# Kernel tuning notes

Measured on AMD Instinct MI355X. Metric: run time of the kernel, lower is better.

The kernel has to match this reference:

```python
import jax, jax.numpy as jnp
import numpy as np

NUM_GRAPHS = 256   # number of graph blocks in the batch
NODES = 64         # nodes per graph (PPGN uses complete pair set per graph)
C_IN = 64          # nedgeinput
C_OUT = 64         # nedgeoutput
E = NUM_GRAPHS * NODES * NODES  # total pair-edges


def _complete_edge_index():
    # PPGN edge set: all (i, j) node pairs within each graph, sorted lexicographically
    base = np.arange(NUM_GRAPHS, dtype=np.int32) * NODES
    ii = np.repeat(np.arange(NODES, dtype=np.int32), NODES)
    jj = np.tile(np.arange(NODES, dtype=np.int32), NODES)
    src = (base[:, None] + ii[None, :]).reshape(-1)
    dst = (base[:, None] + jj[None, :]).reshape(-1)
    return jnp.asarray(np.stack([src, dst]), dtype=jnp.int32)  # [2, E]


def setup_inputs() -> dict:
    key = jax.random.key(0)
    k1, k2, k3, k4 = jax.random.split(key, 4)
    edge_index = _complete_edge_index()
    SP = jax.random.normal(k1, (E, C_IN), dtype=jnp.float32)
    s = 1.0 / np.sqrt(C_IN).astype(np.float32)
    W4 = jax.random.normal(k2, (C_IN, C_IN), dtype=jnp.float32) * s   # fc1_4.weight
    W5 = jax.random.normal(k3, (C_IN, C_IN), dtype=jnp.float32) * s   # fc1_5.weight
    W6 = jax.random.normal(k4, (C_OUT, 2 * C_IN), dtype=jnp.float32) * (1.0 / np.sqrt(2 * C_IN).astype(np.float32))  # fc1_6.weight
    return {"edge_index": edge_index, "SP": SP, "W4": W4, "W5": W5, "W6": W6}


def reference(edge_index, SP, W4, W5, W6):
    # X = fc1_4(SP)/C, Y = fc1_5(SP)/C  (torch Linear: x @ W.T)
    X = (SP @ W4.T) / C_IN   # [E, C]
    Y = (SP @ W5.T) / C_IN   # [E, C]
    # block-diagonal sparse matmul per channel, restricted back to the edge pattern
    g = edge_index[0] // NODES   # graph id per edge
    il = edge_index[0] % NODES   # local row index
    jl = edge_index[1] % NODES   # local col index
    Xd = jnp.zeros((NUM_GRAPHS, NODES, NODES, C_IN), X.dtype).at[g, il, jl].set(X)
    Yd = jnp.zeros((NUM_GRAPHS, NODES, NODES, C_IN), Y.dtype).at[g, il, jl].set(Y)
    prod = jnp.einsum('bikc,bkjc->bijc', Xd, Yd)  # per-graph, per-channel matmul X @ Y
    mm = prod[g, il, jl]                           # gather back to edge list: [E, C]
    tmp = jnp.concatenate([SP, mm], axis=1)        # [E, 2C]
    return jax.nn.relu(tmp @ W6.T)                 # [E, C_OUT]
```

## Files before the change

kernel.cpp:

```cpp
#include <hip/hip_runtime.h>
#include <stdint.h>

#define NG   256
#define NN   64
#define NEDGE (NG*NN*NN)

using bf8   = __attribute__((ext_vector_type(8))) short;
using f32x4 = __attribute__((ext_vector_type(4))) float;

__device__ __forceinline__ unsigned short f2bf(float f) {
  uint32_t u = __float_as_uint(f);
  u += 0x7fffu + ((u >> 16) & 1u);
  return (unsigned short)(u >> 16);
}
__device__ __forceinline__ bf8 pk8(float4 a, float4 b) {
  bf8 r;
  r[0]=(short)f2bf(a.x); r[1]=(short)f2bf(a.y); r[2]=(short)f2bf(a.z); r[3]=(short)f2bf(a.w);
  r[4]=(short)f2bf(b.x); r[5]=(short)f2bf(b.y); r[6]=(short)f2bf(b.z); r[7]=(short)f2bf(b.w);
  return r;
}
__device__ __forceinline__ bf8 ld8bf(const float* p) {
  const float4* q = reinterpret_cast<const float4*>(p);
  return pk8(q[0], q[1]);
}
__device__ __forceinline__ bf8 u4_to_bf8(uint4 v) {
  union { uint4 u; bf8 b; } c; c.u = v; return c.b;
}

__global__ __launch_bounds__(256) void k1_xy(
    const float* __restrict__ SP, const float* __restrict__ W4,
    const float* __restrict__ W5, unsigned short* __restrict__ Xp,
    unsigned short* __restrict__ Yp)
{
  __shared__ unsigned short Wl[2][64*72];
  __shared__ unsigned short lT[2][64*72];
  const int t = threadIdx.x, w = t >> 6, lane = t & 63;
  const int lr = lane & 15, lg = lane >> 4;
  const size_t b = blockIdx.x >> 2;
  const int iq = (int)blockIdx.x & 3;

  {
    const int mat = t >> 7, row = (t >> 1) & 63, h = t & 1;
    const float* src = (mat ? W5 : W4) + row*64 + h*32;
    unsigned short* dst = Wl[mat] + row*72 + h*32;
#pragma unroll
    for (int q = 0; q < 4; ++q) {
      bf8 v = ld8bf(src + q*8);
      *reinterpret_cast<bf8*>(dst + q*8) = v;
    }
  }

#define SPADDR(it_) (SP + ((size_t)b*4096 + (size_t)(iq*16+(it_))*64 + w*16 + lr)*64 + lg*8)
#define PRELOAD(P0_,P1_,P2_,P3_, it_)                                        \
  { const float4* q = reinterpret_cast<const float4*>(SPADDR(it_));          \
    P0_ = q[0]; P1_ = q[1]; P2_ = q[8]; P3_ = q[9]; }

  float4 pA0, pA1, pA2, pA3, pB0, pB1, pB2, pB3;
  PRELOAD(pA0,pA1,pA2,pA3, 0)
  PRELOAD(pB0,pB1,pB2,pB3, 1)
  __syncthreads();

#define WFRAG(mat_, ct_, kk_)                                                \
  (*reinterpret_cast<const bf8*>(Wl[mat_] + ((ct_)*16 + lr)*72 + (kk_)*32 + lg*8))

  const float s = 0.015625f;
#define K1_W1(arr_, ct_, r_, v_)                                             \
  lT[arr_][((ct_)*16 + lg*4 + (r_))*72 + w*16 + lr] = f2bf((v_)*s);
#define K1_W(ct_, ax_, ay_)                                                  \
  K1_W1(0,ct_,0,ax_[0]) K1_W1(0,ct_,1,ax_[1])                                \
  K1_W1(0,ct_,2,ax_[2]) K1_W1(0,ct_,3,ax_[3])                                \
  K1_W1(1,ct_,0,ay_[0]) K1_W1(1,ct_,1,ay_[1])                                \
  K1_W1(1,ct_,2,ay_[2]) K1_W1(1,ct_,3,ay_[3])

#define K1_ITER(it_, P0_,P1_,P2_,P3_, NEXT_)                                 \
  {                                                                          \
    bf8 a0 = pk8(P0_, P1_);                                                  \
    bf8 a1 = pk8(P2_, P3_);                                                  \
    NEXT_                                                                    \
    f32x4 ax0={0.f,0.f,0.f,0.f}, ax1=ax0, ax2=ax0, ax3=ax0;                  \
    f32x4 ay0=ax0, ay1=ax0, ay2=ax0, ay3=ax0;                                \
    ax0 = __builtin_amdgcn_mfma_f32_16x16x32_bf16(WFRAG(0,0,0), a0, ax0,0,0,0);\
    ax0 = __builtin_amdgcn_mfma_f32_16x16x32_bf16(WFRAG(0,0,1), a1, ax0,0,0,0);\
    ay0 = __builtin_amdgcn_mfma_f32_16x16x32_bf16(WFRAG(1,0,0), a0, ay0,0,0,0);\
    ay0 = __builtin_amdgcn_mfma_f32_16x16x32_bf16(WFRAG(1,0,1), a1, ay0,0,0,0);\
    ax1 = __builtin_amdgcn_mfma_f32_16x16x32_bf16(WFRAG(0,1,0), a0, ax1,0,0,0);\
    ax1 = __builtin_amdgcn_mfma_f32_16x16x32_bf16(WFRAG(0,1,1), a1, ax1,0,0,0);\
    ay1 = __builtin_amdgcn_mfma_f32_16x16x32_bf16(WFRAG(1,1,0), a0, ay1,0,0,0);\
    ay1 = __builtin_amdgcn_mfma_f32_16x16x32_bf16(WFRAG(1,1,1), a1, ay1,0,0,0);\
    ax2 = __builtin_amdgcn_mfma_f32_16x16x32_bf16(WFRAG(0,2,0), a0, ax2,0,0,0);\
    ax2 = __builtin_amdgcn_mfma_f32_16x16x32_bf16(WFRAG(0,2,1), a1, ax2,0,0,0);\
    ay2 = __builtin_amdgcn_mfma_f32_16x16x32_bf16(WFRAG(1,2,0), a0, ay2,0,0,0);\
    ay2 = __builtin_amdgcn_mfma_f32_16x16x32_bf16(WFRAG(1,2,1), a1, ay2,0,0,0);\
    ax3 = __builtin_amdgcn_mfma_f32_16x16x32_bf16(WFRAG(0,3,0), a0, ax3,0,0,0);\
    ax3 = __builtin_amdgcn_mfma_f32_16x16x32_bf16(WFRAG(0,3,1), a1, ax3,0,0,0);\
    ay3 = __builtin_amdgcn_mfma_f32_16x16x32_bf16(WFRAG(1,3,0), a0, ay3,0,0,0);\
    ay3 = __builtin_amdgcn_mfma_f32_16x16x32_bf16(WFRAG(1,3,1), a1, ay3,0,0,0);\
    K1_W(0, ax0, ay0) K1_W(1, ax1, ay1) K1_W(2, ax2, ay2) K1_W(3, ax3, ay3)  \
    __syncthreads();                                                         \
    {                                                                        \
      const int jo = t & 7, rid = t >> 3;                                    \
      const int irow8 = (iq*16 + (it_)) * 8;                                 \
      _Pragma("unroll")                                                      \
      for (int q = 0; q < 4; ++q) {                                          \
        int row = q*32 + rid;                                                \
        int a = row >> 6, ch = row & 63;                                     \
        const unsigned short* p = lT[a] + ch*72 + jo*8;                      \
        uint2 lo = *reinterpret_cast<const uint2*>(p);                       \
        uint2 hi = *reinterpret_cast<const uint2*>(p + 4);                   \
        uint4 v; v.x = lo.x; v.y = lo.y; v.z = hi.x; v.w = hi.y;             \
        uint4* G = reinterpret_cast<uint4*>(a ? Yp : Xp);                    \
        G[(b*64 + ch)*512 + irow8 + jo] = v;                                 \
      }                                                                      \
    }                                                                        \
    __syncthreads();                                                         \
  }

#pragma unroll 1
  for (int st = 0; st < 8; ++st) {
    const int itA = st*2, itB = st*2 + 1;
    K1_ITER(itA, pA0,pA1,pA2,pA3,
            if (st < 7) { PRELOAD(pA0,pA1,pA2,pA3, itA+2) })
    K1_ITER(itB, pB0,pB1,pB2,pB3,
            if (st < 7) { PRELOAD(pB0,pB1,pB2,pB3, itB+2) })
  }
}

__global__ __launch_bounds__(256) void k2_mfma(
    const unsigned short* __restrict__ Xp, const unsigned short* __restrict__ Yp,
    unsigned short* __restrict__ mmh)
{
  __shared__ unsigned short Ys[2][64*68];
  __shared__ unsigned short Ds[2][64*68];
  const int t = threadIdx.x, w = t >> 6, lane = t & 63;
  const int lr = lane & 15, lg = lane >> 4;
  const int bid = ((int)blockIdx.x & 7) * 1024 + ((int)blockIdx.x >> 3);
  const int pw = w >> 1;
  const int mh = w & 1;
  const int plane = bid*2 + pw;

  {
    const uint4* Yg = reinterpret_cast<const uint4*>(Yp) + (size_t)plane*512;
    unsigned short* ys = Ys[pw];
    const int kk = lane >> 3, jo = lane & 7;
#pragma unroll
    for (int it = 0; it < 4; ++it) {
      int row = mh*32 + it*8 + kk;
      uint4 v = Yg[row*8 + jo];
      *reinterpret_cast<uint2*>(ys + row*68 + jo*8)     = make_uint2(v.x, v.y);
      *reinterpret_cast<uint2*>(ys + row*68 + jo*8 + 4) = make_uint2(v.z, v.w);
    }
  }
  __syncthreads();

  const unsigned short* ys = Ys[pw];
#define K2_BF(bv_, nt_, kt_)                                                 \
  bf8 bv_;                                                                   \
  bv_[0] = (short)ys[((kt_)*32 + lg*8 + 0)*68 + (nt_)*16 + lr];              \
  bv_[1] = (short)ys[((kt_)*32 + lg*8 + 1)*68 + (nt_)*16 + lr];              \
  bv_[2] = (short)ys[((kt_)*32 + lg*8 + 2)*68 + (nt_)*16 + lr];              \
  bv_[3] = (short)ys[((kt_)*32 + lg*8 + 3)*68 + (nt_)*16 + lr];              \
  bv_[4] = (short)ys[((kt_)*32 + lg*8 + 4)*68 + (nt_)*16 + lr];              \
  bv_[5] = (short)ys[((kt_)*32 + lg*8 + 5)*68 + (nt_)*16 + lr];              \
  bv_[6] = (short)ys[((kt_)*32 + lg*8 + 6)*68 + (nt_)*16 + lr];              \
  bv_[7] = (short)ys[((kt_)*32 + lg*8 + 7)*68 + (nt_)*16 + lr];
  K2_BF(b00, 0, 0) K2_BF(b01, 0, 1)
  K2_BF(b10, 1, 0) K2_BF(b11, 1, 1)
  K2_BF(b20, 2, 0) K2_BF(b21, 2, 1)
  K2_BF(b30, 3, 0) K2_BF(b31, 3, 1)

  const uint4* Xg = reinterpret_cast<const uint4*>(Xp) + (size_t)plane*512;
  f32x4 c00={0.f,0.f,0.f,0.f}, c01=c00, c02=c00, c03=c00;
  f32x4 c10=c00, c11=c00, c12=c00, c13=c00;
#define K2_MT(mt_, c0_, c1_, c2_, c3_)                                       \
  {                                                                          \
    int row = mh*32 + (mt_)*16 + lr;                                         \
    bf8 alo = u4_to_bf8(Xg[row*8 + lg]);                                     \
    bf8 ahi = u4_to_bf8(Xg[row*8 + 4 + lg]);                                 \
    c0_ = __builtin_amdgcn_mfma_f32_16x16x32_bf16(alo, b00, c0_, 0, 0, 0);   \
    c0_ = __builtin_amdgcn_mfma_f32_16x16x32_bf16(ahi, b01, c0_, 0, 0, 0);   \
    c1_ = __builtin_amdgcn_mfma_f32_16x16x32_bf16(alo, b10, c1_, 0, 0, 0);   \
    c1_ = __builtin_amdgcn_mfma_f32_16x16x32_bf16(ahi, b11, c1_, 0, 0, 0);   \
    c2_ = __builtin_amdgcn_mfma_f32_16x16x32_bf16(alo, b20, c2_, 0, 0, 0);   \
    c2_ = __builtin_amdgcn_mfma_f32_16x16x32_bf16(ahi, b21, c2_, 0, 0, 0);   \
    c3_ = __builtin_amdgcn_mfma_f32_16x16x32_bf16(alo, b30, c3_, 0, 0, 0);   \
    c3_ = __builtin_amdgcn_mfma_f32_16x16x32_bf16(ahi, b31, c3_, 0, 0, 0);   \
  }
  K2_MT(0, c00, c01, c02, c03)
  K2_MT(1, c10, c11, c12, c13)

  unsigned short* ds = Ds[pw];
#define K2_D1(mt_, nt_, r_, v_)                                              \
  ds[(mh*32 + (mt_)*16 + lg*4 + (r_))*68 + (nt_)*16 + lr] = f2bf(v_);
#define K2_D(mt_, nt_, c_)                                                   \
  K2_D1(mt_,nt_,0,c_[0]) K2_D1(mt_,nt_,1,c_[1])                              \
  K2_D1(mt_,nt_,2,c_[2]) K2_D1(mt_,nt_,3,c_[3])
  K2_D(0,0,c00) K2_D(0,1,c01) K2_D(0,2,c02) K2_D(0,3,c03)
  K2_D(1,0,c10) K2_D(1,1,c11) K2_D(1,2,c12) K2_D(1,3,c13)
  __syncthreads();

  {
    uint4* Mg = reinterpret_cast<uint4*>(mmh);
    const unsigned short* dsr = Ds[pw];
    const int kk = lane >> 3, jo = lane & 7;
    const int bb = plane >> 6, cc = plane & 63;
#pragma unroll
    for (int it = 0; it < 4; ++it) {
      int row = mh*32 + it*8 + kk;
      uint2 lo = *reinterpret_cast<const uint2*>(dsr + row*68 + jo*8);
      uint2 hi = *reinterpret_cast<const uint2*>(dsr + row*68 + jo*8 + 4);
      uint4 v; v.x = lo.x; v.y = lo.y; v.z = hi.x; v.w = hi.y;
      Mg[((size_t)bb*256 + row*4 + (jo>>1))*128 + cc*2 + (jo&1)] = v;
    }
  }
}

__global__ __launch_bounds__(256) void k3_out(
    const float* __restrict__ SP, const unsigned short* __restrict__ mmh,
    const float* __restrict__ W6, float* __restrict__ out)
{
  __shared__ unsigned short lw[64*140];
  const int t = threadIdx.x, w = t >> 6, lane = t & 63;
  const int lr = lane & 15, lg = lane >> 4;
  const size_t b = blockIdx.x >> 2;
  const int iq = (int)blockIdx.x & 3;

  {
    const int row = t >> 2, seg = t & 3;
    const float* src = W6 + row*128 + seg*32;
    unsigned short* dst = lw + row*140 + seg*32;
#pragma unroll
    for (int q = 0; q < 4; ++q) {
      bf8 v = ld8bf(src + q*8);
      *reinterpret_cast<bf8*>(dst + q*8) = v;
    }
  }

#define K3_E(idx_) (b*4096 + (size_t)(iq*16 + ((idx_)>>2)*4 + w)*64 + ((idx_)&3)*16 + lr)
#define PRELOAD3(P0_,P1_,P2_,P3_, idx_)                                      \
  { const float4* q = reinterpret_cast<const float4*>(SP + K3_E(idx_)*64 + lg*8); \
    P0_ = q[0]; P1_ = q[1]; P2_ = q[8]; P3_ = q[9]; }
#define MMLOAD(m2_, m3_, idx_)                                               \
  { const unsigned short* tp = mmh + (K3_E(idx_) >> 4)*1024 + lg*128 + lr;   \
    m2_[0]=(short)tp[0];    m2_[1]=(short)tp[16];                            \
    m2_[2]=(short)tp[32];   m2_[3]=(short)tp[48];                            \
    m2_[4]=(short)tp[64];   m2_[5]=(short)tp[80];                            \
    m2_[6]=(short)tp[96];   m2_[7]=(short)tp[112];                           \
    m3_[0]=(short)tp[512];  m3_[1]=(short)tp[528];                           \
    m3_[2]=(short)tp[544];  m3_[3]=(short)tp[560];                           \
    m3_[4]=(short)tp[576];  m3_[5]=(short)tp[592];                           \
    m3_[6]=(short)tp[608];  m3_[7]=(short)tp[624]; }

  float4 pA0, pA1, pA2, pA3, pB0, pB1, pB2, pB3;
  bf8 m2A, m3A, m2B, m3B;
  PRELOAD3(pA0,pA1,pA2,pA3, 0)
  PRELOAD3(pB0,pB1,pB2,pB3, 1)
  MMLOAD(m2A, m3A, 0)
  MMLOAD(m2B, m3B, 1)
  __syncthreads();

#define W6F(ct_, kt_)                                                        \
  (*reinterpret_cast<const bf8*>(lw + ((ct_)*16 + lr)*140 + (kt_)*32 + lg*8))

#define K3_ITER(idx_, P0_,P1_,P2_,P3_, M2_, M3_, NEXT_)                      \
  {                                                                          \
    bf8 a0 = pk8(P0_, P1_);                                                  \
    bf8 a1 = pk8(P2_, P3_);                                                  \
    bf8 a2 = M2_;                                                            \
    bf8 a3 = M3_;                                                            \
    NEXT_                                                                    \
    f32x4 c0={0.f,0.f,0.f,0.f}, c1=c0, c2=c0, c3=c0;                         \
    c0 = __builtin_amdgcn_mfma_f32_16x16x32_bf16(W6F(0,0), a0, c0, 0,0,0);   \
    c0 = __builtin_amdgcn_mfma_f32_16x16x32_bf16(W6F(0,1), a1, c0, 0,0,0);   \
    c0 = __builtin_amdgcn_mfma_f32_16x16x32_bf16(W6F(0,2), a2, c0, 0,0,0);   \
    c0 = __builtin_amdgcn_mfma_f32_16x16x32_bf16(W6F(0,3), a3, c0, 0,0,0);   \
    c1 = __builtin_amdgcn_mfma_f32_16x16x32_bf16(W6F(1,0), a0, c1, 0,0,0);   \
    c1 = __builtin_amdgcn_mfma_f32_16x16x32_bf16(W6F(1,1), a1, c1, 0,0,0);   \
    c1 = __builtin_amdgcn_mfma_f32_16x16x32_bf16(W6F(1,2), a2, c1, 0,0,0);   \
    c1 = __builtin_amdgcn_mfma_f32_16x16x32_bf16(W6F(1,3), a3, c1, 0,0,0);   \
    c2 = __builtin_amdgcn_mfma_f32_16x16x32_bf16(W6F(2,0), a0, c2, 0,0,0);   \
    c2 = __builtin_amdgcn_mfma_f32_16x16x32_bf16(W6F(2,1), a1, c2, 0,0,0);   \
    c2 = __builtin_amdgcn_mfma_f32_16x16x32_bf16(W6F(2,2), a2, c2, 0,0,0);   \
    c2 = __builtin_amdgcn_mfma_f32_16x16x32_bf16(W6F(2,3), a3, c2, 0,0,0);   \
    c3 = __builtin_amdgcn_mfma_f32_16x16x32_bf16(W6F(3,0), a0, c3, 0,0,0);   \
    c3 = __builtin_amdgcn_mfma_f32_16x16x32_bf16(W6F(3,1), a1, c3, 0,0,0);   \
    c3 = __builtin_amdgcn_mfma_f32_16x16x32_bf16(W6F(3,2), a2, c3, 0,0,0);   \
    c3 = __builtin_amdgcn_mfma_f32_16x16x32_bf16(W6F(3,3), a3, c3, 0,0,0);   \
    float* ob = out + K3_E(idx_)*64 + lg*4;                                  \
    f32x4 o;                                                                 \
    o[0]=fmaxf(c0[0],0.f); o[1]=fmaxf(c0[1],0.f);                            \
    o[2]=fmaxf(c0[2],0.f); o[3]=fmaxf(c0[3],0.f);                            \
    *reinterpret_cast<f32x4*>(ob) = o;                                       \
    o[0]=fmaxf(c1[0],0.f); o[1]=fmaxf(c1[1],0.f);                            \
    o[2]=fmaxf(c1[2],0.f); o[3]=fmaxf(c1[3],0.f);                            \
    *reinterpret_cast<f32x4*>(ob + 16) = o;                                  \
    o[0]=fmaxf(c2[0],0.f); o[1]=fmaxf(c2[1],0.f);                            \
    o[2]=fmaxf(c2[2],0.f); o[3]=fmaxf(c2[3],0.f);                            \
    *reinterpret_cast<f32x4*>(ob + 32) = o;                                  \
    o[0]=fmaxf(c3[0],0.f); o[1]=fmaxf(c3[1],0.f);                            \
    o[2]=fmaxf(c3[2],0.f); o[3]=fmaxf(c3[3],0.f);                            \
    *reinterpret_cast<f32x4*>(ob + 48) = o;                                  \
  }

#pragma unroll 1
  for (int st = 0; st < 8; ++st) {
    const int idxA = st*2, idxB = st*2 + 1;
    K3_ITER(idxA, pA0,pA1,pA2,pA3, m2A, m3A,
            if (st < 7) { PRELOAD3(pA0,pA1,pA2,pA3, idxA+2)
                          MMLOAD(m2A, m3A, idxA+2) })
    K3_ITER(idxB, pB0,pB1,pB2,pB3, m2B, m3B,
            if (st < 7) { PRELOAD3(pB0,pB1,pB2,pB3, idxB+2)
                          MMLOAD(m2B, m3B, idxB+2) })
  }
}

extern "C" void kernel_launch(void* const* d_in, const int* in_sizes, int n_in,
                              void* d_out, int out_size, void* d_ws, size_t ws_size,
                              hipStream_t stream)
{
  (void)in_sizes; (void)n_in; (void)out_size; (void)ws_size;
  const float* SP = (const float*)d_in[1];
  const float* W4 = (const float*)d_in[2];
  const float* W5 = (const float*)d_in[3];
  const float* W6 = (const float*)d_in[4];

  unsigned short* Xp = (unsigned short*)d_out;
  unsigned short* Yp = Xp + (size_t)NEDGE * 64;
  unsigned short* mmh = (unsigned short*)d_ws;
  float* out = (float*)d_out;

  k1_xy  <<<NG*4,     256, 0, stream>>>(SP, W4, W5, Xp, Yp);
  k2_mfma<<<NG*32,    256, 0, stream>>>(Xp, Yp, mmh);
  k3_out <<<NG*4,     256, 0, stream>>>(SP, mmh, W6, out);
}
```

Baseline: 337.9 us.

## Warp-specialize output kernel with producer waves staging SP through double-buffered LDS

Splits the final projection kernel into 512-thread blocks where four waves convert SP rows to bf16 into a double-buffered shared tile while four other waves load the mm tile and run the MFMA projection with ReLU. The goal is to overlap SP global loads and conversion with compute, and to coalesce SP loads. In exchange, only half the waves do MFMA work, and a block-wide barrier is added at every step.

```diff
diff --git a/kernel.cpp b/kernel.cpp
--- a/kernel.cpp
+++ b/kernel.cpp
@@ -214,33 +214,39 @@
   }
 }
 
-__global__ __launch_bounds__(256) void k3_out(
+__global__ __launch_bounds__(512) void k3_out(
     const float* __restrict__ SP, const unsigned short* __restrict__ mmh,
     const float* __restrict__ W6, float* __restrict__ out)
 {
+  __shared__ unsigned short lsp[2][64*72];
   __shared__ unsigned short lw[64*140];
   const int t = threadIdx.x, w = t >> 6, lane = t & 63;
   const int lr = lane & 15, lg = lane >> 4;
-  const size_t b = blockIdx.x >> 2;
-  const int iq = (int)blockIdx.x & 3;
+  const size_t base_e = (size_t)blockIdx.x * 512;
 
   {
-    const int row = t >> 2, seg = t & 3;
-    const float* src = W6 + row*128 + seg*32;
-    unsigned short* dst = lw + row*140 + seg*32;
-#pragma unroll
-    for (int q = 0; q < 4; ++q) {
-      bf8 v = ld8bf(src + q*8);
-      *reinterpret_cast<bf8*>(dst + q*8) = v;
-    }
-  }
-
-#define K3_E(idx_) (b*4096 + (size_t)(iq*16 + ((idx_)>>2)*4 + w)*64 + ((idx_)&3)*16 + lr)
-#define PRELOAD3(P0_,P1_,P2_,P3_, idx_)                                      \
-  { const float4* q = reinterpret_cast<const float4*>(SP + K3_E(idx_)*64 + lg*8); \
-    P0_ = q[0]; P1_ = q[1]; P2_ = q[8]; P3_ = q[9]; }
-#define MMLOAD(m2_, m3_, idx_)                                               \
-  { const unsigned short* tp = mmh + (K3_E(idx_) >> 4)*1024 + lg*128 + lr;   \
+    const int row = t >> 3, seg = t & 7;
+    bf8 v = ld8bf(W6 + row*128 + seg*16);
+    bf8 v2 = ld8bf(W6 + row*128 + seg*16 + 8);
+    *reinterpret_cast<bf8*>(lw + row*140 + seg*16) = v;
+    *reinterpret_cast<bf8*>(lw + row*140 + seg*16 + 8) = v2;
+  }
+
+#define PRODUCE(t_, buf_)                                                    \
+  {                                                                          \
+    const int e0 = t >> 3, seg = t & 7;                                      \
+    const float* s0 = SP + (base_e + (t_)*64 + e0)*64 + seg*8;               \
+    bf8 v0 = ld8bf(s0);                                                      \
+    const float* s1 = s0 + (size_t)32*64;                                    \
+    bf8 v1 = ld8bf(s1);                                                      \
+    *reinterpret_cast<bf8*>(&lsp[buf_][e0*72 + seg*8]) = v0;                 \
+    *reinterpret_cast<bf8*>(&lsp[buf_][(e0+32)*72 + seg*8]) = v1;            \
+  }
+
+  const int sub = w - 4;
+#define MMLOAD(m2_, m3_, t_)                                                 \
+  { const unsigned short* tp = mmh +                                         \
+        ((size_t)blockIdx.x*32 + (t_)*4 + sub)*1024 + lg*128 + lr;           \
     m2_[0]=(short)tp[0];    m2_[1]=(short)tp[16];                            \
     m2_[2]=(short)tp[32];   m2_[3]=(short)tp[48];                            \
     m2_[4]=(short)tp[64];   m2_[5]=(short)tp[80];                            \
@@ -250,24 +256,16 @@
     m3_[4]=(short)tp[576];  m3_[5]=(short)tp[592];                           \
     m3_[6]=(short)tp[608];  m3_[7]=(short)tp[624]; }
 
-  float4 pA0, pA1, pA2, pA3, pB0, pB1, pB2, pB3;
-  bf8 m2A, m3A, m2B, m3B;
-  PRELOAD3(pA0,pA1,pA2,pA3, 0)
-  PRELOAD3(pB0,pB1,pB2,pB3, 1)
-  MMLOAD(m2A, m3A, 0)
-  MMLOAD(m2B, m3B, 1)
-  __syncthreads();
-
 #define W6F(ct_, kt_)                                                        \
   (*reinterpret_cast<const bf8*>(lw + ((ct_)*16 + lr)*140 + (kt_)*32 + lg*8))
 
-#define K3_ITER(idx_, P0_,P1_,P2_,P3_, M2_, M3_, NEXT_)                      \
+#define CONSUME(t_, buf_, M2_, M3_)                                          \
   {                                                                          \
-    bf8 a0 = pk8(P0_, P1_);                                                  \
-    bf8 a1 = pk8(P2_, P3_);                                                  \
+    const unsigned short* sp = &lsp[buf_][(sub*16 + lr)*72 + lg*8];          \
+    bf8 a0 = *reinterpret_cast<const bf8*>(sp);                              \
+    bf8 a1 = *reinterpret_cast<const bf8*>(sp + 32);                         \
     bf8 a2 = M2_;                                                            \
     bf8 a3 = M3_;                                                            \
-    NEXT_                                                                    \
     f32x4 c0={0.f,0.f,0.f,0.f}, c1=c0, c2=c0, c3=c0;                         \
     c0 = __builtin_amdgcn_mfma_f32_16x16x32_bf16(W6F(0,0), a0, c0, 0,0,0);   \
     c0 = __builtin_amdgcn_mfma_f32_16x16x32_bf16(W6F(0,1), a1, c0, 0,0,0);   \
@@ -285,7 +283,7 @@
     c3 = __builtin_amdgcn_mfma_f32_16x16x32_bf16(W6F(3,1), a1, c3, 0,0,0);   \
     c3 = __builtin_amdgcn_mfma_f32_16x16x32_bf16(W6F(3,2), a2, c3, 0,0,0);   \
     c3 = __builtin_amdgcn_mfma_f32_16x16x32_bf16(W6F(3,3), a3, c3, 0,0,0);   \
-    float* ob = out + K3_E(idx_)*64 + lg*4;                                  \
+    float* ob = out + (base_e + (t_)*64 + sub*16 + lr)*64 + lg*4;            \
     f32x4 o;                                                                 \
     o[0]=fmaxf(c0[0],0.f); o[1]=fmaxf(c0[1],0.f);                            \
     o[2]=fmaxf(c0[2],0.f); o[3]=fmaxf(c0[3],0.f);                            \
@@ -301,15 +299,31 @@
     *reinterpret_cast<f32x4*>(ob + 48) = o;                                  \
   }
 
+  bf8 m2A, m3A, m2B, m3B;
+  if (w < 4) {
+    PRODUCE(0, 0)
+  } else {
+    MMLOAD(m2A, m3A, 0)
+  }
+  __syncthreads();
+
 #pragma unroll 1
-  for (int st = 0; st < 8; ++st) {
-    const int idxA = st*2, idxB = st*2 + 1;
-    K3_ITER(idxA, pA0,pA1,pA2,pA3, m2A, m3A,
-            if (st < 7) { PRELOAD3(pA0,pA1,pA2,pA3, idxA+2)
-                          MMLOAD(m2A, m3A, idxA+2) })
-    K3_ITER(idxB, pB0,pB1,pB2,pB3, m2B, m3B,
-            if (st < 7) { PRELOAD3(pB0,pB1,pB2,pB3, idxB+2)
-                          MMLOAD(m2B, m3B, idxB+2) })
+  for (int st = 0; st < 4; ++st) {
+    const int t0 = st*2, t1 = st*2 + 1;
+    if (w < 4) {
+      PRODUCE(t0 + 1, (t0 + 1) & 1)
+    } else {
+      MMLOAD(m2B, m3B, t1)
+      CONSUME(t0, t0 & 1, m2A, m3A)
+    }
+    __syncthreads();
+    if (w < 4) {
+      if (st < 3) { PRODUCE(t1 + 1, (t1 + 1) & 1) }
+    } else {
+      if (st < 3) { MMLOAD(m2A, m3A, t1 + 1) }
+      CONSUME(t1, t1 & 1, m2B, m3B)
+    }
+    __syncthreads();
   }
 }
 
@@ -330,5 +344,5 @@
 
   k1_xy  <<<NG*4,     256, 0, stream>>>(SP, W4, W5, Xp, Yp);
   k2_mfma<<<NG*32,    256, 0, stream>>>(Xp, Yp, mmh);
-  k3_out <<<NG*4,     256, 0, stream>>>(SP, mmh, W6, out);
-}
+  k3_out <<<NEDGE/512, 512, 0, stream>>>(SP, mmh, W6, out);
+}
```

Result: faster. 331.1 us (-2.0%).

## Stage SP tiles into LDS via async global_load_lds with double buffering in k3

Applied to the files above, without the earlier changes.

The output kernel now copies SP rows straight into a double-buffered LDS tile using global_load_lds DMA instead of holding them in registers through per-thread float4 loads. Each block processes a contiguous range of 1024 edges, and the copy of the next tile is issued while the current one is being multiplied. The aim is to cut register pressure and make the global reads coalesced and overlapped. In exchange it adds 32KB of LDS per block, which can lower occupancy, plus two block-wide barriers per tile. The layout remapping is subtle, so correctness depends on the DMA lane addressing matching the consumer indexing.

```diff
diff --git a/kernel.cpp b/kernel.cpp
--- a/kernel.cpp
+++ b/kernel.cpp
@@ -218,11 +218,11 @@
     const float* __restrict__ SP, const unsigned short* __restrict__ mmh,
     const float* __restrict__ W6, float* __restrict__ out)
 {
+  __shared__ float lsp[2][64*64];
   __shared__ unsigned short lw[64*140];
   const int t = threadIdx.x, w = t >> 6, lane = t & 63;
   const int lr = lane & 15, lg = lane >> 4;
-  const size_t b = blockIdx.x >> 2;
-  const int iq = (int)blockIdx.x & 3;
+  const size_t base_e = (size_t)blockIdx.x * 1024;
 
   {
     const int row = t >> 2, seg = t & 3;
@@ -235,12 +235,22 @@
     }
   }
 
-#define K3_E(idx_) (b*4096 + (size_t)(iq*16 + ((idx_)>>2)*4 + w)*64 + ((idx_)&3)*16 + lr)
-#define PRELOAD3(P0_,P1_,P2_,P3_, idx_)                                      \
-  { const float4* q = reinterpret_cast<const float4*>(SP + K3_E(idx_)*64 + lg*8); \
-    P0_ = q[0]; P1_ = q[1]; P2_ = q[8]; P3_ = q[9]; }
-#define MMLOAD(m2_, m3_, idx_)                                               \
-  { const unsigned short* tp = mmh + (K3_E(idx_) >> 4)*1024 + lg*128 + lr;   \
+#define K3DMA(tt_, buf_)                                                     \
+  _Pragma("unroll")                                                          \
+  for (int d = 0; d < 4; ++d) {                                              \
+    const int u = d*4 + w;                                                   \
+    const int oe = u*32 + (lane >> 1);                                       \
+    const float* src = SP + (base_e + (size_t)(tt_)*64 + (oe & 63))*64       \
+                          + (oe >> 6)*8 + (lane & 1)*4;                      \
+    __builtin_amdgcn_global_load_lds(                                        \
+        (const __attribute__((address_space(1))) unsigned int*)src,          \
+        (__attribute__((address_space(3))) unsigned int*)&lsp[buf_][u*256],  \
+        16, 0, 0);                                                           \
+  }
+
+#define MMLOAD(m2_, m3_, tt_)                                                \
+  { const unsigned short* tp = mmh +                                         \
+        ((size_t)blockIdx.x*64 + (tt_)*4 + w)*1024 + lg*128 + lr;            \
     m2_[0]=(short)tp[0];    m2_[1]=(short)tp[16];                            \
     m2_[2]=(short)tp[32];   m2_[3]=(short)tp[48];                            \
     m2_[4]=(short)tp[64];   m2_[5]=(short)tp[80];                            \
@@ -250,24 +260,16 @@
     m3_[4]=(short)tp[576];  m3_[5]=(short)tp[592];                           \
     m3_[6]=(short)tp[608];  m3_[7]=(short)tp[624]; }
 
-  float4 pA0, pA1, pA2, pA3, pB0, pB1, pB2, pB3;
-  bf8 m2A, m3A, m2B, m3B;
-  PRELOAD3(pA0,pA1,pA2,pA3, 0)
-  PRELOAD3(pB0,pB1,pB2,pB3, 1)
-  MMLOAD(m2A, m3A, 0)
-  MMLOAD(m2B, m3B, 1)
-  __syncthreads();
-
 #define W6F(ct_, kt_)                                                        \
   (*reinterpret_cast<const bf8*>(lw + ((ct_)*16 + lr)*140 + (kt_)*32 + lg*8))
 
-#define K3_ITER(idx_, P0_,P1_,P2_,P3_, M2_, M3_, NEXT_)                      \
+#define CONSUME(tt_, buf_, M2_, M3_)                                         \
   {                                                                          \
-    bf8 a0 = pk8(P0_, P1_);                                                  \
-    bf8 a1 = pk8(P2_, P3_);                                                  \
+    const int e = w*16 + lr;                                                 \
+    bf8 a0 = ld8bf(&lsp[buf_][(lg*64 + e)*8]);             \
+    bf8 a1 = ld8bf(&lsp[buf_][((4 + lg)*64 + e)*8]);    \
     bf8 a2 = M2_;                                                            \
     bf8 a3 = M3_;                                                            \
-    NEXT_                                                                    \
     f32x4 c0={0.f,0.f,0.f,0.f}, c1=c0, c2=c0, c3=c0;                         \
     c0 = __builtin_amdgcn_mfma_f32_16x16x32_bf16(W6F(0,0), a0, c0, 0,0,0);   \
     c0 = __builtin_amdgcn_mfma_f32_16x16x32_bf16(W6F(0,1), a1, c0, 0,0,0);   \
@@ -285,7 +287,7 @@
     c3 = __builtin_amdgcn_mfma_f32_16x16x32_bf16(W6F(3,1), a1, c3, 0,0,0);   \
     c3 = __builtin_amdgcn_mfma_f32_16x16x32_bf16(W6F(3,2), a2, c3, 0,0,0);   \
     c3 = __builtin_amdgcn_mfma_f32_16x16x32_bf16(W6F(3,3), a3, c3, 0,0,0);   \
-    float* ob = out + K3_E(idx_)*64 + lg*4;                                  \
+    float* ob = out + (base_e + (size_t)(tt_)*64 + e)*64 + lg*4;             \
     f32x4 o;                                                                 \
     o[0]=fmaxf(c0[0],0.f); o[1]=fmaxf(c0[1],0.f);                            \
     o[2]=fmaxf(c0[2],0.f); o[3]=fmaxf(c0[3],0.f);                            \
@@ -301,15 +303,24 @@
     *reinterpret_cast<f32x4*>(ob + 48) = o;                                  \
   }
 
+  bf8 m2A, m3A, m2B, m3B;
+  K3DMA(0, 0)
+  MMLOAD(m2A, m3A, 0)
+  __syncthreads();
+
 #pragma unroll 1
   for (int st = 0; st < 8; ++st) {
-    const int idxA = st*2, idxB = st*2 + 1;
-    K3_ITER(idxA, pA0,pA1,pA2,pA3, m2A, m3A,
-            if (st < 7) { PRELOAD3(pA0,pA1,pA2,pA3, idxA+2)
-                          MMLOAD(m2A, m3A, idxA+2) })
-    K3_ITER(idxB, pB0,pB1,pB2,pB3, m2B, m3B,
-            if (st < 7) { PRELOAD3(pB0,pB1,pB2,pB3, idxB+2)
-                          MMLOAD(m2B, m3B, idxB+2) })
+    const int t0 = st*2, t1 = t0 + 1;
+    K3DMA(t1, 1)
+    MMLOAD(m2B, m3B, t1)
+    CONSUME(t0, 0, m2A, m3A)
+    __syncthreads();
+    if (st < 7) {
+      K3DMA(t1 + 1, 0)
+      MMLOAD(m2A, m3A, t1 + 1)
+    }
+    CONSUME(t1, 1, m2B, m3B)
+    __syncthreads();
   }
 }
 
@@ -328,7 +339,7 @@
   unsigned short* mmh = (unsigned short*)d_ws;
   float* out = (float*)d_out;
 
-  k1_xy  <<<NG*4,     256, 0, stream>>>(SP, W4, W5, Xp, Yp);
-  k2_mfma<<<NG*32,    256, 0, stream>>>(Xp, Yp, mmh);
-  k3_out <<<NG*4,     256, 0, stream>>>(SP, mmh, W6, out);
-}
+  k1_xy  <<<NG*4,      256, 0, stream>>>(SP, W4, W5, Xp, Yp);
+  k2_mfma<<<NG*32,     256, 0, stream>>>(Xp, Yp, mmh);
+  k3_out <<<NEDGE/1024, 256, 0, stream>>>(SP, mmh, W6, out);
+}
```

Measured after the change: 344.3 us. Within noise of the previous version (+1.9%).
